# Optimization experiments

Measured on AMD Instinct MI355X. Metric: run time of the kernel, lower is better.

The kernel has to match this reference:

```python
import jax, jax.numpy as jnp
import numpy as np

N_HEADS = 8
KEY_DIM = 64
MEM_DIM = 64
HEAD_DIM = 64
IN_DIM = 256
OUT_DIM = 256


def setup_inputs() -> dict:
    key = jax.random.key(0)
    ks = jax.random.split(key, 7)
    x = jax.random.normal(ks[0], (8, IN_DIM, 64, 64), dtype=jnp.float32)
    # learned params
    key_p = jax.random.uniform(ks[1], (N_HEADS, KEY_DIM, MEM_DIM), dtype=jnp.float32)
    memory = jax.random.uniform(ks[2], (N_HEADS, MEM_DIM, HEAD_DIM), dtype=jnp.float32) * 0.5 - 0.25
    w_in = jax.random.normal(ks[3], (N_HEADS * KEY_DIM, IN_DIM), dtype=jnp.float32) * (1.0 / np.sqrt(IN_DIM))
    b_in = jax.random.normal(ks[4], (N_HEADS * KEY_DIM,), dtype=jnp.float32) * 0.01
    w_out = jax.random.normal(ks[5], (OUT_DIM, N_HEADS * HEAD_DIM), dtype=jnp.float32) * (1.0 / np.sqrt(N_HEADS * HEAD_DIM))
    b_out = jax.random.normal(ks[6], (OUT_DIM,), dtype=jnp.float32) * 0.01
    return {"x": x, "key_p": key_p, "memory": memory, "w_in": w_in, "b_in": b_in, "w_out": w_out, "b_out": b_out}


def reference(x, key_p, memory, w_in, b_in, w_out, b_out):
    B, _, H, W = x.shape
    # 1x1 conv projection: [B, n_heads*key_dim, H, W]
    out = jnp.einsum('oc,bchw->bohw', w_in, x) + b_in[None, :, None, None]
    # split heads: b (k n) h w -> b n k h w  (einops '(c m)' with m=n_heads => c is outer)
    out = out.reshape(B, KEY_DIM, N_HEADS, H, W).transpose(0, 2, 1, 3, 4)
    # per-head key matmul over key_dim -> memory_dim
    out = jnp.einsum('nkm,bnkhw->bnmhw', key_p, out)
    out = jax.nn.softmax(out, axis=2)
    # per-head memory matmul over memory_dim -> head_dim
    out = jnp.einsum('nmd,bnmhw->bndhw', memory, out)
    # merge heads: b n d h w -> b (d n) h w  (einops 'b m c h w -> b (m c) h w' with m=heads... wait)
    # einops 'b m c h w -> b (m c) h w': m (heads) is outer -> transpose then reshape
    out = out.reshape(B, N_HEADS * HEAD_DIM, H, W)
    # final 1x1 conv
    out = jnp.einsum('oc,bchw->bohw', w_out, out) + b_out[None, :, None, None]
    return out
```

## Files before the change

### kernel.cpp

```cpp
#include <hip/hip_runtime.h>


typedef _Float16 half8 __attribute__((ext_vector_type(8)));
typedef _Float16 half4 __attribute__((ext_vector_type(4)));
typedef _Float16 half2v __attribute__((ext_vector_type(2)));
typedef float float4v __attribute__((ext_vector_type(4)));

__global__ void fold_a(const float* __restrict__ key_p, const float* __restrict__ w_in,
                       const float* __restrict__ b_in, _Float16* __restrict__ Aswz,
                       float* __restrict__ bb) {
    int row = blockIdx.x;
    int c   = threadIdx.x;
    int n = row >> 6, m = row & 63;
    float v = 0.f;
    for (int k = 0; k < 64; ++k)
        v += key_p[n * 4096 + k * 64 + m] * w_in[(k * 8 + n) * 256 + c];
    int R = row >> 4, s = c >> 5, i = c & 7, lsub = (c >> 3) & 3;
    int l = (row & 15) + 16 * lsub;
    Aswz[(((R * 8 + s) * 64 + l) << 3) + i] = (_Float16)v;
    if (c == 0) {
        float s2 = 0.f;
        for (int k = 0; k < 64; ++k)
            s2 += key_p[n * 4096 + k * 64 + m] * b_in[k * 8 + n];
        bb[row] = s2;
    }
}

__global__ void fold_m(const float* __restrict__ w_out, const float* __restrict__ memory,
                       _Float16* __restrict__ Mswz) {
    int o = blockIdx.x;
    int t = threadIdx.x;
    for (int hh = 0; hh < 2; ++hh) {
        int col = t + hh * 256;
        int n = col >> 6, m = col & 63;
        float v = 0.f;
        for (int d = 0; d < 64; ++d)
            v += w_out[o * 512 + n * 64 + d] * memory[n * 4096 + m * 64 + d];
        int R2 = o >> 4, s = col >> 5, i = col & 7;
        int l = (o & 15) + 16 * ((col >> 3) & 3);
        Mswz[(((R2 * 16 + s) * 64 + l) << 3) + i] = (_Float16)v;
    }
}

#define XS_STRIDE 264
#define PR_STRIDE 520

__global__ __launch_bounds__(256, 2) void fused_main(
    const float* __restrict__ x, const _Float16* __restrict__ Aswz,
    const float* __restrict__ bb, const _Float16* __restrict__ Mswz,
    const float* __restrict__ b_out, float* __restrict__ out)
{
    __shared__ _Float16 S[64 * PR_STRIDE];

    const int t  = threadIdx.x;
    const int w  = t >> 6;
    const int l  = t & 63;
    const int q  = l >> 4;
    const int lp = l & 15;
    const int wg  = blockIdx.x;
    const int b   = wg >> 6;
    const int hw0 = (wg & 63) * 64;
    const float* xb = x + (size_t)b * 256 * 4096 + hw0;

    #pragma unroll
    for (int i = 0; i < 8; ++i) {
        int u  = i * 256 + t;
        int cp = u & 127;
        int qq = u >> 7;
        int c0 = cp * 2, p4 = qq * 4;
        const float* px = xb + (size_t)c0 * 4096 + p4;
        float4 v0 = *(const float4*)(px);
        float4 v1 = *(const float4*)(px + 4096);
        *(half2v*)(&S[(p4 + 0) * XS_STRIDE + c0]) = half2v{(_Float16)v0.x, (_Float16)v1.x};
        *(half2v*)(&S[(p4 + 1) * XS_STRIDE + c0]) = half2v{(_Float16)v0.y, (_Float16)v1.y};
        *(half2v*)(&S[(p4 + 2) * XS_STRIDE + c0]) = half2v{(_Float16)v0.z, (_Float16)v1.z};
        *(half2v*)(&S[(p4 + 3) * XS_STRIDE + c0]) = half2v{(_Float16)v0.w, (_Float16)v1.w};
    }
    __syncthreads();

    float4v acc[8][4];
    #pragma unroll
    for (int r = 0; r < 8; ++r)
        #pragma unroll
        for (int c = 0; c < 4; ++c) acc[r][c] = float4v{0.f, 0.f, 0.f, 0.f};

    const half8* Ag = (const half8*)Aswz;
    for (int s = 0; s < 8; ++s) {
        half8 bf[4];
        #pragma unroll
        for (int c = 0; c < 4; ++c)
            bf[c] = *(const half8*)(&S[(c * 16 + lp) * XS_STRIDE + s * 32 + q * 8]);
        half8 af[8];
        #pragma unroll
        for (int r = 0; r < 8; ++r)
            af[r] = Ag[((w * 8 + r) * 8 + s) * 64 + l];
        #pragma unroll
        for (int r = 0; r < 8; ++r)
            #pragma unroll
            for (int c = 0; c < 4; ++c)
                acc[r][c] = __builtin_amdgcn_mfma_f32_16x16x32_f16(af[r], bf[c], acc[r][c], 0, 0, 0);
    }

    #pragma unroll
    for (int r = 0; r < 8; ++r) {
        float4v bbv = *(const float4v*)(bb + w * 128 + r * 16 + q * 4);
        #pragma unroll
        for (int c = 0; c < 4; ++c)
            #pragma unroll
            for (int j = 0; j < 4; ++j) acc[r][c][j] += bbv[j];
    }

    __syncthreads();

    #pragma unroll
    for (int h = 0; h < 2; ++h) {
        #pragma unroll
        for (int c = 0; c < 4; ++c) {
            float mx = -1e30f;
            #pragma unroll
            for (int rr = 0; rr < 4; ++rr) {
                int r = h * 4 + rr;
                #pragma unroll
                for (int j = 0; j < 4; ++j) mx = fmaxf(mx, acc[r][c][j]);
            }
            mx = fmaxf(mx, __shfl_xor(mx, 16, 64));
            mx = fmaxf(mx, __shfl_xor(mx, 32, 64));
            float sum = 0.f;
            #pragma unroll
            for (int rr = 0; rr < 4; ++rr) {
                int r = h * 4 + rr;
                #pragma unroll
                for (int j = 0; j < 4; ++j) {
                    float e = __expf(acc[r][c][j] - mx);
                    acc[r][c][j] = e;
                    sum += e;
                }
            }
            sum += __shfl_xor(sum, 16, 64);
            sum += __shfl_xor(sum, 32, 64);
            float inv = 1.f / sum;
            #pragma unroll
            for (int rr = 0; rr < 4; ++rr) {
                int r = h * 4 + rr;
                half4 pv = {(_Float16)(acc[r][c][0] * inv), (_Float16)(acc[r][c][1] * inv),
                            (_Float16)(acc[r][c][2] * inv), (_Float16)(acc[r][c][3] * inv)};
                *(half4*)(&S[(c * 16 + lp) * PR_STRIDE + w * 128 + r * 16 + q * 4]) = pv;
            }
        }
    }
    __syncthreads();

    float4v acc2[4][4];
    #pragma unroll
    for (int r = 0; r < 4; ++r)
        #pragma unroll
        for (int c = 0; c < 4; ++c) acc2[r][c] = float4v{0.f, 0.f, 0.f, 0.f};

    const half8* Mg = (const half8*)Mswz;
    for (int s2 = 0; s2 < 16; ++s2) {
        half8 bf2[4];
        #pragma unroll
        for (int c = 0; c < 4; ++c)
            bf2[c] = *(const half8*)(&S[(c * 16 + lp) * PR_STRIDE + s2 * 32 + q * 8]);
        half8 af2[4];
        #pragma unroll
        for (int r = 0; r < 4; ++r)
            af2[r] = Mg[((w * 4 + r) * 16 + s2) * 64 + l];
        #pragma unroll
        for (int r = 0; r < 4; ++r)
            #pragma unroll
            for (int c = 0; c < 4; ++c)
                acc2[r][c] = __builtin_amdgcn_mfma_f32_16x16x32_f16(af2[r], bf2[c], acc2[r][c], 0, 0, 0);
    }

    #pragma unroll
    for (int r = 0; r < 4; ++r) {
        int ob = w * 64 + r * 16 + q * 4;
        float4v bo = *(const float4v*)(b_out + ob);
        #pragma unroll
        for (int j = 0; j < 4; ++j) {
            float* orow = out + ((size_t)b * 256 + ob + j) * 4096 + hw0;
            #pragma unroll
            for (int c = 0; c < 4; ++c)
                orow[c * 16 + lp] = acc2[r][c][j] + bo[j];
        }
    }
}

extern "C" void kernel_launch(void* const* d_in, const int* in_sizes, int n_in,
                              void* d_out, int out_size, void* d_ws, size_t ws_size,
                              hipStream_t stream) {
    (void)in_sizes; (void)n_in; (void)ws_size; (void)out_size;
    const float* x      = (const float*)d_in[0];
    const float* key_p  = (const float*)d_in[1];
    const float* memory = (const float*)d_in[2];
    const float* w_in   = (const float*)d_in[3];
    const float* b_in   = (const float*)d_in[4];
    const float* w_out  = (const float*)d_in[5];
    const float* b_out  = (const float*)d_in[6];
    float* out = (float*)d_out;

    _Float16* Aswz = (_Float16*)d_ws;
    _Float16* Mswz = Aswz + 512 * 256;
    float*    bb   = (float*)(Mswz + 256 * 512);

    fold_a<<<512, 256, 0, stream>>>(key_p, w_in, b_in, Aswz, bb);
    fold_m<<<256, 256, 0, stream>>>(w_out, memory, Mswz);
    fused_main<<<512, 256, 0, stream>>>(x, Aswz, bb, Mswz, b_out, out);
}
```

Before: 131.7 us.

## Merge weight-folding kernels and swizzle softmax probabilities in shared memory

The two weight-folding kernels become one launch. Each block stages its shared operand (a key_p column or a w_out row) in LDS, and the memory rows are read with float4 loads. In the main kernel the softmax probability tile moves from a padded row-major layout to an MFMA-fragment-swizzled layout, so each lane reads its B fragment as one contiguous half8. This also shrinks shared memory from 66 KB to 64 KB per block. The aim is to cut one launch, speed up the folding work and reduce LDS bank conflicts and footprint, at the risk of conflicts on the new half4 writes.

After: 120.2 us. -8.8%, faster.

```diff
diff --git a/kernel.cpp b/kernel.cpp
--- a/kernel.cpp
+++ b/kernel.cpp
@@ -6,51 +6,67 @@
 typedef _Float16 half2v __attribute__((ext_vector_type(2)));
 typedef float float4v __attribute__((ext_vector_type(4)));
 
-__global__ void fold_a(const float* __restrict__ key_p, const float* __restrict__ w_in,
-                       const float* __restrict__ b_in, _Float16* __restrict__ Aswz,
-                       float* __restrict__ bb) {
-    int row = blockIdx.x;
-    int c   = threadIdx.x;
-    int n = row >> 6, m = row & 63;
-    float v = 0.f;
-    for (int k = 0; k < 64; ++k)
-        v += key_p[n * 4096 + k * 64 + m] * w_in[(k * 8 + n) * 256 + c];
-    int R = row >> 4, s = c >> 5, i = c & 7, lsub = (c >> 3) & 3;
-    int l = (row & 15) + 16 * lsub;
-    Aswz[(((R * 8 + s) * 64 + l) << 3) + i] = (_Float16)v;
-    if (c == 0) {
-        float s2 = 0.f;
+__global__ __launch_bounds__(256) void fold_all(
+    const float* __restrict__ key_p, const float* __restrict__ w_in,
+    const float* __restrict__ b_in, const float* __restrict__ w_out,
+    const float* __restrict__ memory,
+    _Float16* __restrict__ Aswz, _Float16* __restrict__ Mswz, float* __restrict__ bb)
+{
+    __shared__ float sv[512];
+    __shared__ float red[64];
+    const int blk = blockIdx.x;
+    const int t = threadIdx.x;
+
+    if (blk < 512) {
+        const int row = blk, n = row >> 6, m = row & 63;
+        if (t < 64) sv[t] = key_p[n * 4096 + t * 64 + m];
+        __syncthreads();
+        const int c = t;
+        float v = 0.f;
+        #pragma unroll 8
         for (int k = 0; k < 64; ++k)
-            s2 += key_p[n * 4096 + k * 64 + m] * b_in[k * 8 + n];
-        bb[row] = s2;
+            v = fmaf(sv[k], w_in[(k * 8 + n) * 256 + c], v);
+        int R = row >> 4, s = c >> 5, i = c & 7;
+        int l = (row & 15) + 16 * ((c >> 3) & 3);
+        Aswz[(((R * 8 + s) * 64 + l) << 3) + i] = (_Float16)v;
+        if (t < 64) red[t] = sv[t] * b_in[t * 8 + n];
+        __syncthreads();
+        if (t == 0) {
+            float s2 = 0.f;
+            for (int k = 0; k < 64; ++k) s2 += red[k];
+            bb[row] = s2;
+        }
+    } else {
+        const int o = blk - 512;
+        sv[t]       = w_out[o * 512 + t];
+        sv[256 + t] = w_out[o * 512 + 256 + t];
+        __syncthreads();
+        #pragma unroll
+        for (int hh = 0; hh < 2; ++hh) {
+            int col = t + hh * 256, n = col >> 6, m = col & 63;
+            const float4* mrow = (const float4*)(memory + n * 4096 + m * 64);
+            const float4* wrow = (const float4*)(sv + n * 64);
+            float v = 0.f;
+            #pragma unroll
+            for (int qd = 0; qd < 16; ++qd) {
+                float4 a = mrow[qd], w = wrow[qd];
+                v += a.x * w.x + a.y * w.y + a.z * w.z + a.w * w.w;
+            }
+            int R2 = o >> 4, s = col >> 5, i = col & 7;
+            int l = (o & 15) + 16 * ((col >> 3) & 3);
+            Mswz[(((R2 * 16 + s) * 64 + l) << 3) + i] = (_Float16)v;
+        }
     }
 }
 
-__global__ void fold_m(const float* __restrict__ w_out, const float* __restrict__ memory,
-                       _Float16* __restrict__ Mswz) {
-    int o = blockIdx.x;
-    int t = threadIdx.x;
-    for (int hh = 0; hh < 2; ++hh) {
-        int col = t + hh * 256;
-        int n = col >> 6, m = col & 63;
-        float v = 0.f;
-        for (int d = 0; d < 64; ++d)
-            v += w_out[o * 512 + n * 64 + d] * memory[n * 4096 + m * 64 + d];
-        int R2 = o >> 4, s = col >> 5, i = col & 7;
-        int l = (o & 15) + 16 * ((col >> 3) & 3);
-        Mswz[(((R2 * 16 + s) * 64 + l) << 3) + i] = (_Float16)v;
-    }
-}
-
 #define XS_STRIDE 264
-#define PR_STRIDE 520
 
 __global__ __launch_bounds__(256, 2) void fused_main(
     const float* __restrict__ x, const _Float16* __restrict__ Aswz,
     const float* __restrict__ bb, const _Float16* __restrict__ Mswz,
     const float* __restrict__ b_out, float* __restrict__ out)
 {
-    __shared__ _Float16 S[64 * PR_STRIDE];
+    __shared__ _Float16 S[32768];
 
     const int t  = threadIdx.x;
     const int w  = t >> 6;
@@ -142,9 +158,12 @@
             #pragma unroll
             for (int rr = 0; rr < 4; ++rr) {
                 int r = h * 4 + rr;
+                int s2 = w * 4 + (r >> 1);
+                int lq = ((r & 1) * 2 + (q >> 1)) * 16 + lp;
+                int i0 = (q & 1) * 4;
                 half4 pv = {(_Float16)(acc[r][c][0] * inv), (_Float16)(acc[r][c][1] * inv),
                             (_Float16)(acc[r][c][2] * inv), (_Float16)(acc[r][c][3] * inv)};
-                *(half4*)(&S[(c * 16 + lp) * PR_STRIDE + w * 128 + r * 16 + q * 4]) = pv;
+                *(half4*)(&S[(((s2 * 4 + c) * 64) + lq) * 8 + i0]) = pv;
             }
         }
     }
@@ -161,7 +180,7 @@
         half8 bf2[4];
         #pragma unroll
         for (int c = 0; c < 4; ++c)
-            bf2[c] = *(const half8*)(&S[(c * 16 + lp) * PR_STRIDE + s2 * 32 + q * 8]);
+            bf2[c] = *(const half8*)(&S[(((s2 * 4 + c) * 64) + l) * 8]);
         half8 af2[4];
         #pragma unroll
         for (int r = 0; r < 4; ++r)
@@ -204,7 +223,6 @@
     _Float16* Mswz = Aswz + 512 * 256;
     float*    bb   = (float*)(Mswz + 256 * 512);
 
-    fold_a<<<512, 256, 0, stream>>>(key_p, w_in, b_in, Aswz, bb);
-    fold_m<<<256, 256, 0, stream>>>(w_out, memory, Mswz);
+    fold_all<<<768, 256, 0, stream>>>(key_p, w_in, b_in, w_out, memory, Aswz, Mswz, bb);
     fused_main<<<512, 256, 0, stream>>>(x, Aswz, bb, Mswz, b_out, out);
 }
```
